# Performance work log

Hardware: AMD Instinct MI355X
Metric: run time of the kernel (lower is better)

Reference implementation:

```python
import jax, jax.numpy as jnp
import numpy as np

N, E, D, L = 50000, 800000, 64, 4
ATOM_VOCAB, BOND_VOCAB, N_ATOM_F, N_BOND_F = 64, 8, 9, 3
BN_EPS = 1e-5


def _bn_train(z, g, b):
    # BatchNorm1d in training mode: batch mean, biased variance
    mu = jnp.mean(z, axis=0)
    var = jnp.mean((z - mu) ** 2, axis=0)
    return (z - mu) * jax.lax.rsqrt(var + BN_EPS) * g + b


def _multi_embed(tables, idx):
    # tables: [F, V, D], idx: [N, F] -> sum over F of tables[f][idx[:, f]] -> [N, D]
    return jax.vmap(lambda t, c: t[c], in_axes=(0, 1))(tables, idx).sum(0)


def setup_inputs() -> dict:
    key = jax.random.key(0)
    ks = jax.random.split(key, 8)
    s = 0.1
    return {
        "x": jax.random.randint(ks[0], (N, N_ATOM_F), 0, ATOM_VOCAB),
        "edge_index": jax.random.randint(ks[1], (2, E), 0, N),
        "edge_attr": jax.random.randint(ks[2], (E, N_BOND_F), 0, BOND_VOCAB),
        "atom_emb": jax.random.normal(ks[3], (N_ATOM_F, ATOM_VOCAB, D), jnp.float32) * s,
        "bond_emb": jax.random.normal(ks[4], (L, N_BOND_F, BOND_VOCAB, D), jnp.float32) * s,
        "lin1_w": jax.random.normal(ks[5], (L, D, 2 * D), jnp.float32) * s,
        "lin1_b": jnp.zeros((L, 2 * D), jnp.float32),
        "bn1_g": jnp.ones((L, 2 * D), jnp.float32),
        "bn1_b": jnp.zeros((L, 2 * D), jnp.float32),
        "lin2_w": jax.random.normal(ks[6], (L, 2 * D, D), jnp.float32) * s,
        "lin2_b": jnp.zeros((L, D), jnp.float32),
        "eps": jnp.zeros((L,), jnp.float32),
        "bn_g": jnp.ones((L, D), jnp.float32),
        "bn_b": jnp.zeros((L, D), jnp.float32),
    }


def reference(x, edge_index, edge_attr, atom_emb, bond_emb, lin1_w, lin1_b,
              bn1_g, bn1_b, lin2_w, lin2_b, eps, bn_g, bn_b):
    n_nodes = x.shape[0]
    n_layers = lin1_w.shape[0]
    src, dst = edge_index[0], edge_index[1]
    # AtomEncoder: sum of per-feature embeddings
    h = _multi_embed(atom_emb, x)  # [N, D]
    for l in range(n_layers):
        e = _multi_embed(bond_emb[l], edge_attr)  # [E, D] bond encoding
        msg = jax.nn.relu(h[src] + e)  # gather + elementwise message
        agg = jax.ops.segment_sum(msg, dst, num_segments=n_nodes)  # scatter-add
        z = (1.0 + eps[l]) * h + agg  # GIN update
        z = jax.nn.relu(_bn_train(z @ lin1_w[l] + lin1_b[l], bn1_g[l], bn1_b[l]))
        z = z @ lin2_w[l] + lin2_b[l]
        h = _bn_train(z, bn_g[l], bn_b[l])  # outer BatchNorm
        if l < n_layers - 1:
            h = jax.nn.relu(h)
    return h  # JK='last' node representation [N, D]
```

## Files before the change

kernel.cpp:

```cpp
#include <hip/hip_runtime.h>
#include <hip/hip_bf16.h>

#define NN 50000
#define NE 800000
#define NAF 9
#define NBF 3
#define BN_EPS 1e-5f
#define NBUK 196
#define CHUNK 8192
#define NTILE 3125
#define MMB 1563

typedef __attribute__((ext_vector_type(8))) short bf16x8;
typedef __attribute__((ext_vector_type(4))) float f32x4;

__device__ __forceinline__ short f2b(float f) {
  unsigned u = __float_as_uint(f);
  unsigned r = (u + 0x7FFFu + ((u >> 16) & 1u)) >> 16;
  return (short)r;
}

__device__ __forceinline__ float b2f(unsigned short v) {
  return __uint_as_float(((unsigned)v) << 16);
}

__device__ __forceinline__ bf16x8 pack8(float4 a, float4 b) {
  bf16x8 v;
  v[0] = f2b(a.x); v[1] = f2b(a.y); v[2] = f2b(a.z); v[3] = f2b(a.w);
  v[4] = f2b(b.x); v[5] = f2b(b.y); v[6] = f2b(b.z); v[7] = f2b(b.w);
  return v;
}

__global__ __launch_bounds__(256) void k_atom(const int* __restrict__ x,
                                              const float* __restrict__ aemb,
                                              float* __restrict__ h,
                                              unsigned short* __restrict__ hb) {
  int node = (blockIdx.x * 256 + threadIdx.x) >> 6;
  int lane = threadIdx.x & 63;
  if (node >= NN) return;
  const int* xr = x + node * NAF;
  float acc = 0.f;
#pragma unroll
  for (int f = 0; f < NAF; ++f) acc += aemb[(f * 64 + xr[f]) * 64 + lane];
  h[(size_t)node * 64 + lane] = acc;
  hb[(size_t)node * 64 + lane] = (unsigned short)f2b(acc);
}

__global__ __launch_bounds__(256) void k_prep(const float* __restrict__ w1,
                                              const float* __restrict__ w2,
                                              bf16x8* __restrict__ pre1,
                                              bf16x8* __restrict__ pre2) {
  int f = (blockIdx.x & 15) * 256 + threadIdx.x;
  int lane = f & 63, c = lane & 15, g = lane >> 4;
  if (blockIdx.x < 16) {
    int kh = (f >> 6) & 1, t = (f >> 7) & 7, l = f >> 10;
    const float* w = w1 + (size_t)l * 64 * 128;
    bf16x8 v;
#pragma unroll
    for (int j = 0; j < 8; ++j) v[j] = f2b(w[(kh * 32 + g * 8 + j) * 128 + t * 16 + c]);
    pre1[f] = v;
  } else {
    int kf = (f >> 6) & 3, t = (f >> 8) & 3, l = f >> 10;
    const float* w = w2 + (size_t)l * 128 * 64;
    bf16x8 v;
#pragma unroll
    for (int j = 0; j < 8; ++j) v[j] = f2b(w[(kf * 32 + g * 8 + j) * 64 + t * 16 + c]);
    pre2[f] = v;
  }
}

__global__ __launch_bounds__(256) void k_red(const float* __restrict__ partial,
                                             float* __restrict__ st, int width) {
  int col = threadIdx.x;
  if (col >= width) return;
  int per = (MMB + gridDim.x - 1) / gridDim.x;
  int r0 = blockIdx.x * per;
  int r1 = min(MMB, r0 + per);
  float s = 0.f;
  int r = r0;
  for (; r + 4 <= r1; r += 4) {
    s += partial[(size_t)r * width + col] + partial[(size_t)(r + 1) * width + col]
       + partial[(size_t)(r + 2) * width + col] + partial[(size_t)(r + 3) * width + col];
  }
  for (; r < r1; ++r) s += partial[(size_t)r * width + col];
  atomicAdd(&st[col], s);
}

__global__ __launch_bounds__(256) void k_hprep(float* __restrict__ zB,
                                               const float* __restrict__ st,
                                               const float* __restrict__ g,
                                               const float* __restrict__ b,
                                               unsigned short* __restrict__ hb) {
  __shared__ float ns[64], nbv[64];
  if (threadIdx.x < 64) {
    int c = threadIdx.x;
    const float inv = 1.0f / NN;
    float mu = st[c] * inv;
    float var = st[64 + c] * inv - mu * mu;
    float sc = rsqrtf(var + BN_EPS) * g[c];
    ns[c] = sc;
    nbv[c] = b[c] - mu * sc;
  }
  __syncthreads();
  float4* z4 = (float4*)zB;
  ushort4* hb4 = (ushort4*)hb;
  int total = NN * 16;
  for (int i = blockIdx.x * 256 + threadIdx.x; i < total; i += gridDim.x * 256) {
    float4 v = z4[i];
    int c = (i & 15) * 4;
    v.x = fmaxf(fmaf(v.x, ns[c], nbv[c]), 0.f);
    v.y = fmaxf(fmaf(v.y, ns[c + 1], nbv[c + 1]), 0.f);
    v.z = fmaxf(fmaf(v.z, ns[c + 2], nbv[c + 2]), 0.f);
    v.w = fmaxf(fmaf(v.w, ns[c + 3], nbv[c + 3]), 0.f);
    z4[i] = v;
    ushort4 o;
    o.x = (unsigned short)f2b(v.x);
    o.y = (unsigned short)f2b(v.y);
    o.z = (unsigned short)f2b(v.z);
    o.w = (unsigned short)f2b(v.w);
    hb4[i] = o;
  }
}

__global__ __launch_bounds__(1024) void k_pack_hist(const int* __restrict__ ei,
                                                    const int* __restrict__ ea,
                                                    uint2* __restrict__ pairs,
                                                    int* __restrict__ counts,
                                                    int* __restrict__ bcnt) {
  __shared__ int lh[NBUK];
  for (int i = threadIdx.x; i < NBUK; i += 1024) lh[i] = 0;
  __syncthreads();
  for (int e = blockIdx.x * 1024 + threadIdx.x; e < NE; e += gridDim.x * 1024) {
    int src = ei[e];
    int dst = ei[NE + e];
    unsigned code = (unsigned)(ea[e * 3] | (ea[e * 3 + 1] << 3) | (ea[e * 3 + 2] << 6));
    pairs[e] = make_uint2((unsigned)src | (code << 17), (unsigned)dst);
    atomicAdd(&counts[dst], 1);
    atomicAdd(&lh[dst >> 8], 1);
  }
  __syncthreads();
  for (int i = threadIdx.x; i < NBUK; i += 1024)
    if (lh[i]) atomicAdd(&bcnt[i], lh[i]);
}

__global__ __launch_bounds__(256) void k_scanb(const int* __restrict__ bcnt,
                                               int* __restrict__ bbase,
                                               int* __restrict__ bfill) {
  int tid = threadIdx.x;
  int c = (tid < NBUK) ? bcnt[tid] : 0;
  int lane = tid & 63, wid = tid >> 6;
  int inc = c;
#pragma unroll
  for (int off = 1; off < 64; off <<= 1) {
    int t = __shfl_up(inc, off);
    if (lane >= off) inc += t;
  }
  __shared__ int wt[4];
  if (lane == 63) wt[wid] = inc;
  __syncthreads();
  int woff = 0;
#pragma unroll
  for (int w = 0; w < 4; ++w) woff += (w < wid) ? wt[w] : 0;
  if (tid < NBUK) { int e = inc - c + woff; bbase[tid] = e; bfill[tid] = e; }
}

__global__ __launch_bounds__(256) void k_scan1(const int* __restrict__ counts,
                                               int* __restrict__ row_ptr,
                                               int* __restrict__ bsum) {
  int tid = threadIdx.x;
  int node = blockIdx.x * 256 + tid;
  int c = (node < NN) ? counts[node] : 0;
  int lane = tid & 63, wid = tid >> 6;
  int inc = c;
#pragma unroll
  for (int off = 1; off < 64; off <<= 1) {
    int t = __shfl_up(inc, off);
    if (lane >= off) inc += t;
  }
  __shared__ int wt[4];
  if (lane == 63) wt[wid] = inc;
  __syncthreads();
  int woff = 0;
#pragma unroll
  for (int w = 0; w < 4; ++w) woff += (w < wid) ? wt[w] : 0;
  if (node < NN) row_ptr[node] = inc - c + woff;
  if (tid == 255) bsum[blockIdx.x] = woff + inc;
}

__global__ __launch_bounds__(256) void k_scan2(const int* __restrict__ bsum,
                                               int* __restrict__ boff, int nb) {
  int tid = threadIdx.x;
  int c = (tid < nb) ? bsum[tid] : 0;
  int lane = tid & 63, wid = tid >> 6;
  int inc = c;
#pragma unroll
  for (int off = 1; off < 64; off <<= 1) {
    int t = __shfl_up(inc, off);
    if (lane >= off) inc += t;
  }
  __shared__ int wt[4];
  if (lane == 63) wt[wid] = inc;
  __syncthreads();
  int woff = 0;
#pragma unroll
  for (int w = 0; w < 4; ++w) woff += (w < wid) ? wt[w] : 0;
  if (tid < nb) boff[tid] = inc - c + woff;
}

__global__ __launch_bounds__(256) void k_scan3(int* __restrict__ row_ptr,
                                               const int* __restrict__ boff) {
  int node = blockIdx.x * 256 + threadIdx.x;
  if (node < NN) row_ptr[node] += boff[blockIdx.x];
  if (node == 0) row_ptr[NN] = NE;
}

__global__ __launch_bounds__(1024) void k_bin(const uint2* __restrict__ pairs,
                                              int* __restrict__ bfill,
                                              uint2* __restrict__ binned) {
  __shared__ uint2 st[CHUNK];
  __shared__ int lh[NBUK];
  __shared__ int gbase[NBUK];
  int tid = threadIdx.x;
  int base = blockIdx.x * CHUNK;
  int n = NE - base; if (n > CHUNK) n = CHUNK;
  for (int i = tid; i < NBUK; i += 1024) lh[i] = 0;
  __syncthreads();
  for (int i = tid; i < n; i += 1024) {
    uint2 p = pairs[base + i];
    st[i] = p;
    atomicAdd(&lh[p.y >> 8], 1);
  }
  __syncthreads();
  for (int i = tid; i < NBUK; i += 1024) {
    int c = lh[i];
    gbase[i] = c ? atomicAdd(&bfill[i], c) : 0;
  }
  __syncthreads();
  for (int i = tid; i < NBUK; i += 1024) lh[i] = 0;
  __syncthreads();
  for (int i = tid; i < n; i += 1024) {
    uint2 p = st[i];
    int b = p.y >> 8;
    int r = atomicAdd(&lh[b], 1);
    binned[gbase[b] + r] = p;
  }
}

__global__ __launch_bounds__(1024) void k_fin(const uint2* __restrict__ binned,
                                              const int* __restrict__ bbase,
                                              const int* __restrict__ bcnt,
                                              const int* __restrict__ row_ptr,
                                              unsigned* __restrict__ epack) {
  __shared__ int cur[256];
  int b = blockIdx.x;
  int tid = threadIdx.x;
  int node0 = b << 8;
  if (tid < 256) cur[tid] = (node0 + tid < NN) ? row_ptr[node0 + tid] : 0;
  __syncthreads();
  int s = bbase[b], n = bcnt[b];
  for (int i = tid; i < n; i += 1024) {
    uint2 p = binned[s + i];
    int pos = atomicAdd(&cur[p.y & 255], 1);
    epack[pos] = p.x;
  }
}

__global__ __launch_bounds__(256) void k_agg(const float* __restrict__ hf,
                                             const unsigned short* __restrict__ hb,
                                             const float* __restrict__ bemb,
                                             const float* __restrict__ eps, int l,
                                             const int* __restrict__ row_ptr,
                                             const unsigned* __restrict__ epack,
                                             float* __restrict__ z) {
  __shared__ float tab[NBF * 8 * 64];
  const float* bt = bemb + (size_t)l * NBF * 8 * 64;
  for (int i = threadIdx.x; i < NBF * 8 * 64; i += 256) tab[i] = bt[i];
  __syncthreads();
  const float4* tab4 = (const float4*)tab;
  const ushort4* hb4 = (const ushort4*)hb;
  const float4* hf4 = (const float4*)hf;

  int node = (blockIdx.x * 256 + threadIdx.x) >> 6;
  int lane = threadIdx.x & 63;
  if (node >= NN) return;
  int gr = lane >> 4;
  int c4 = lane & 15;

  int beg = row_ptr[node], end = row_ptr[node + 1];
  float4 acc = {0.f, 0.f, 0.f, 0.f};

  auto edge = [&](unsigned p, ushort4 hv) {
    unsigned cd = p >> 17;
    float4 ea_ = tab4[(cd & 7) * 16 + c4];
    float4 eb_ = tab4[128 + ((cd >> 3) & 7) * 16 + c4];
    float4 ec_ = tab4[256 + ((cd >> 6) & 7) * 16 + c4];
    acc.x += fmaxf(b2f(hv.x) + ea_.x + eb_.x + ec_.x, 0.f);
    acc.y += fmaxf(b2f(hv.y) + ea_.y + eb_.y + ec_.y, 0.f);
    acc.z += fmaxf(b2f(hv.z) + ea_.z + eb_.z + ec_.z, 0.f);
    acc.w += fmaxf(b2f(hv.w) + ea_.w + eb_.w + ec_.w, 0.f);
  };

  int i = beg + gr;
  for (; i + 12 < end; i += 16) {
    unsigned p0 = epack[i];
    unsigned p1 = epack[i + 4];
    unsigned p2 = epack[i + 8];
    unsigned p3 = epack[i + 12];
    ushort4 h0 = hb4[(size_t)(p0 & 0x1FFFFu) * 16 + c4];
    ushort4 h1 = hb4[(size_t)(p1 & 0x1FFFFu) * 16 + c4];
    ushort4 h2 = hb4[(size_t)(p2 & 0x1FFFFu) * 16 + c4];
    ushort4 h3 = hb4[(size_t)(p3 & 0x1FFFFu) * 16 + c4];
    edge(p0, h0); edge(p1, h1); edge(p2, h2); edge(p3, h3);
  }
  for (; i < end; i += 4) {
    unsigned p0 = epack[i];
    ushort4 h0 = hb4[(size_t)(p0 & 0x1FFFFu) * 16 + c4];
    edge(p0, h0);
  }
#pragma unroll
  for (int off = 16; off <= 32; off <<= 1) {
    acc.x += __shfl_xor(acc.x, off);
    acc.y += __shfl_xor(acc.y, off);
    acc.z += __shfl_xor(acc.z, off);
    acc.w += __shfl_xor(acc.w, off);
  }
  if (gr == 0) {
    float4 self = hf4[(size_t)node * 16 + c4];
    float se = 1.0f + eps[l];
    float4 out;
    out.x = fmaf(self.x, se, acc.x);
    out.y = fmaf(self.y, se, acc.y);
    out.z = fmaf(self.z, se, acc.z);
    out.w = fmaf(self.w, se, acc.w);
    ((float4*)z)[(size_t)node * 16 + c4] = out;
  }
}

__global__ __launch_bounds__(256) void k_mm1(const float* __restrict__ z,
                                             const bf16x8* __restrict__ pre1,
                                             const float* __restrict__ b1,
                                             int l, float* __restrict__ y,
                                             float* __restrict__ part1) {
  __shared__ float lz[2][16 * 68];
  int tid = threadIdx.x;
  int lane = tid & 63;
  int wid = tid >> 6;
  int c = lane & 15;
  int g = lane >> 4;

  int t0 = blockIdx.x * 2;
  int ntl = (t0 + 1 < NTILE) ? 2 : 1;

  const float4* zt = (const float4*)(z + (size_t)t0 * 16 * 64);
  int nf4 = ntl * 256;
  for (int i = tid; i < nf4; i += 256) {
    float4 v = zt[i];
    int tile = i >> 8;
    int f4 = i & 255;
    int row = f4 >> 4, c4i = f4 & 15;
    *(float4*)(&lz[tile][row * 68 + c4i * 4]) = v;
  }

  bf16x8 Bf[2][2];
#pragma unroll
  for (int u = 0; u < 2; ++u)
#pragma unroll
    for (int kh = 0; kh < 2; ++kh)
      Bf[u][kh] = pre1[(((size_t)l * 8 + wid * 2 + u) * 2 + kh) * 64 + lane];
  float bias0 = b1[l * 128 + (wid * 2) * 16 + c];
  float bias1 = b1[l * 128 + (wid * 2 + 1) * 16 + c];

  __syncthreads();

  float ssum0 = 0.f, ssum1 = 0.f, sq0 = 0.f, sq1 = 0.f;

#pragma unroll
  for (int u = 0; u < 2; ++u) {
    if (u >= ntl) break;
    int rowbase = (t0 + u) * 16;
    const float* myz = lz[u];
    float4 q0 = *(const float4*)(myz + c * 68 + g * 8);
    float4 q1 = *(const float4*)(myz + c * 68 + g * 8 + 4);
    float4 q2 = *(const float4*)(myz + c * 68 + 32 + g * 8);
    float4 q3 = *(const float4*)(myz + c * 68 + 32 + g * 8 + 4);
    bf16x8 a0 = pack8(q0, q1);
    bf16x8 a1 = pack8(q2, q3);

    f32x4 acc0 = {bias0, bias0, bias0, bias0};
    acc0 = __builtin_amdgcn_mfma_f32_16x16x32_bf16(a0, Bf[0][0], acc0, 0, 0, 0);
    acc0 = __builtin_amdgcn_mfma_f32_16x16x32_bf16(a1, Bf[0][1], acc0, 0, 0, 0);
    f32x4 acc1 = {bias1, bias1, bias1, bias1};
    acc1 = __builtin_amdgcn_mfma_f32_16x16x32_bf16(a0, Bf[1][0], acc1, 0, 0, 0);
    acc1 = __builtin_amdgcn_mfma_f32_16x16x32_bf16(a1, Bf[1][1], acc1, 0, 0, 0);

    int tc0 = wid * 2, tc1 = wid * 2 + 1;
#pragma unroll
    for (int r = 0; r < 4; ++r) {
      float v0 = acc0[r], v1 = acc1[r];
      y[(size_t)(rowbase + g * 4 + r) * 128 + tc0 * 16 + c] = v0;
      y[(size_t)(rowbase + g * 4 + r) * 128 + tc1 * 16 + c] = v1;
      ssum0 += v0; sq0 = fmaf(v0, v0, sq0);
      ssum1 += v1; sq1 = fmaf(v1, v1, sq1);
    }
  }
  ssum0 += __shfl_xor(ssum0, 16); ssum0 += __shfl_xor(ssum0, 32);
  ssum1 += __shfl_xor(ssum1, 16); ssum1 += __shfl_xor(ssum1, 32);
  sq0 += __shfl_xor(sq0, 16); sq0 += __shfl_xor(sq0, 32);
  sq1 += __shfl_xor(sq1, 16); sq1 += __shfl_xor(sq1, 32);
  if (g == 0) {
    float* pp = part1 + (size_t)blockIdx.x * 256;
    pp[(wid * 2) * 16 + c] = ssum0;
    pp[(wid * 2 + 1) * 16 + c] = ssum1;
    pp[128 + (wid * 2) * 16 + c] = sq0;
    pp[128 + (wid * 2 + 1) * 16 + c] = sq1;
  }
}

__global__ __launch_bounds__(256) void k_mm2(const float* __restrict__ y,
                                             const bf16x8* __restrict__ pre2,
                                             const float* __restrict__ b2,
                                             const float* __restrict__ g1,
                                             const float* __restrict__ bb1,
                                             int l, float* __restrict__ z2,
                                             const float* __restrict__ st1,
                                             float* __restrict__ part2) {
  __shared__ float ly[2][16 * 132];
  __shared__ float ns[128], nb[128];
  int tid = threadIdx.x;
  int lane = tid & 63;
  int wid = tid >> 6;
  int c = lane & 15;
  int g = lane >> 4;

  int t0 = blockIdx.x * 2;
  int ntl = (t0 + 1 < NTILE) ? 2 : 1;

  const float4* yt = (const float4*)(y + (size_t)t0 * 16 * 128);
  int nf4 = ntl * 512;
  for (int i = tid; i < nf4; i += 256) {
    float4 v = yt[i];
    int tile = i >> 9;
    int f4 = i & 511;
    int row = f4 >> 5, c4i = f4 & 31;
    *(float4*)(&ly[tile][row * 132 + c4i * 4]) = v;
  }

  if (tid < 128) {
    int ch = tid;
    const float inv = 1.0f / NN;
    float mu = st1[ch] * inv;
    float var = st1[128 + ch] * inv - mu * mu;
    float sc = rsqrtf(var + BN_EPS) * g1[l * 128 + ch];
    ns[ch] = sc;
    nb[ch] = bb1[l * 128 + ch] - mu * sc;
  }

  bf16x8 Bf[4];
#pragma unroll
  for (int kf = 0; kf < 4; ++kf)
    Bf[kf] = pre2[(((size_t)l * 4 + wid) * 4 + kf) * 64 + lane];
  float bias = b2[l * 64 + wid * 16 + c];

  __syncthreads();

  const float4* nsf = (const float4*)ns;
  const float4* nbf = (const float4*)nb;
  float ssum = 0.f, sq = 0.f;

#pragma unroll
  for (int u = 0; u < 2; ++u) {
    if (u >= ntl) break;
    int rowbase = (t0 + u) * 16;
    const float* myy = ly[u];
    bf16x8 A[4];
#pragma unroll
    for (int kf = 0; kf < 4; ++kf) {
      float4 q0 = *(const float4*)(myy + c * 132 + kf * 32 + g * 8);
      float4 q1 = *(const float4*)(myy + c * 132 + kf * 32 + g * 8 + 4);
      float4 s0 = nsf[kf * 8 + g * 2];
      float4 s1 = nsf[kf * 8 + g * 2 + 1];
      float4 o0 = nbf[kf * 8 + g * 2];
      float4 o1 = nbf[kf * 8 + g * 2 + 1];
      float4 v0, v1;
      v0.x = fmaxf(fmaf(q0.x, s0.x, o0.x), 0.f);
      v0.y = fmaxf(fmaf(q0.y, s0.y, o0.y), 0.f);
      v0.z = fmaxf(fmaf(q0.z, s0.z, o0.z), 0.f);
      v0.w = fmaxf(fmaf(q0.w, s0.w, o0.w), 0.f);
      v1.x = fmaxf(fmaf(q1.x, s1.x, o1.x), 0.f);
      v1.y = fmaxf(fmaf(q1.y, s1.y, o1.y), 0.f);
      v1.z = fmaxf(fmaf(q1.z, s1.z, o1.z), 0.f);
      v1.w = fmaxf(fmaf(q1.w, s1.w, o1.w), 0.f);
      A[kf] = pack8(v0, v1);
    }
    f32x4 acc = {bias, bias, bias, bias};
#pragma unroll
    for (int kf = 0; kf < 4; ++kf)
      acc = __builtin_amdgcn_mfma_f32_16x16x32_bf16(A[kf], Bf[kf], acc, 0, 0, 0);
#pragma unroll
    for (int r = 0; r < 4; ++r) {
      float v = acc[r];
      z2[(size_t)(rowbase + g * 4 + r) * 64 + wid * 16 + c] = v;
      ssum += v; sq = fmaf(v, v, sq);
    }
  }
  ssum += __shfl_xor(ssum, 16); ssum += __shfl_xor(ssum, 32);
  sq += __shfl_xor(sq, 16); sq += __shfl_xor(sq, 32);
  if (g == 0) {
    float* pp = part2 + (size_t)blockIdx.x * 128;
    pp[wid * 16 + c] = ssum;
    pp[64 + wid * 16 + c] = sq;
  }
}

__global__ __launch_bounds__(256) void k_bn2(const float* __restrict__ z2,
                                             const float* __restrict__ g,
                                             const float* __restrict__ b,
                                             const float* __restrict__ st,
                                             float* __restrict__ h) {
  __shared__ float ns[64], nb[64];
  if (threadIdx.x < 64) {
    int c = threadIdx.x;
    const float inv = 1.0f / NN;
    float mu = st[c] * inv;
    float var = st[64 + c] * inv - mu * mu;
    float sc = rsqrtf(var + BN_EPS) * g[c];
    ns[c] = sc;
    nb[c] = b[c] - mu * sc;
  }
  __syncthreads();
  const float4* zin = (const float4*)z2;
  float4* hout = (float4*)h;
  int total = NN * 16;
  for (int i = blockIdx.x * 256 + threadIdx.x; i < total; i += gridDim.x * 256) {
    float4 v = zin[i];
    int c = (i & 15) * 4;
    v.x = fmaf(v.x, ns[c], nb[c]);
    v.y = fmaf(v.y, ns[c + 1], nb[c + 1]);
    v.z = fmaf(v.z, ns[c + 2], nb[c + 2]);
    v.w = fmaf(v.w, ns[c + 3], nb[c + 3]);
    hout[i] = v;
  }
}

extern "C" void kernel_launch(void* const* d_in, const int* in_sizes, int n_in,
                              void* d_out, int out_size, void* d_ws, size_t ws_size,
                              hipStream_t stream) {
  const int* x = (const int*)d_in[0];
  const int* ei = (const int*)d_in[1];
  const int* ea = (const int*)d_in[2];
  const float* aemb = (const float*)d_in[3];
  const float* bemb = (const float*)d_in[4];
  const float* l1w = (const float*)d_in[5];
  const float* l1b = (const float*)d_in[6];
  const float* g1 = (const float*)d_in[7];
  const float* bb1 = (const float*)d_in[8];
  const float* l2w = (const float*)d_in[9];
  const float* l2b = (const float*)d_in[10];
  const float* eps = (const float*)d_in[11];
  const float* bng = (const float*)d_in[12];
  const float* bnb = (const float*)d_in[13];
  float* out = (float*)d_out;

  char* p = (char*)d_ws;
  float* zA = (float*)p;           p += (size_t)NN * 64 * 4;
  float* y = (float*)p;            p += (size_t)NN * 128 * 4;
  float* zB = (float*)p;           p += (size_t)NN * 64 * 4;
  unsigned* epack = (unsigned*)p;  p += (size_t)NE * 4;
  int* row_ptr = (int*)p;          p += (size_t)(NN + 1) * 4;
  int* counts = (int*)p;           p += (size_t)NN * 4;
  int* bcnt = (int*)p;             p += 256 * 4;
  int* bbase = (int*)p;            p += 256 * 4;
  int* bfill = (int*)p;            p += 256 * 4;
  float* stats = (float*)p;        p += 4 * 384 * 4;
  int* bsum = (int*)p;             p += 256 * 4;
  int* boff = (int*)p;             p += 256 * 4;
  bf16x8* pre1 = (bf16x8*)p;       p += 4096 * 16;
  bf16x8* pre2 = (bf16x8*)p;       p += 4096 * 16;
  float* part1 = (float*)p;        p += (size_t)MMB * 256 * 4;
  float* part2 = (float*)p;        p += (size_t)MMB * 128 * 4;

  uint2* pairs = (uint2*)zA;
  uint2* binned = (uint2*)y;
  unsigned short* hb = (unsigned short*)y;
  float* h0 = zB;

  const int NB = (NN + 255) / 256;

  hipMemsetAsync(counts, 0, (size_t)NN * 4, stream);
  hipMemsetAsync(bcnt, 0, 256 * 4, stream);
  hipMemsetAsync(stats, 0, 4 * 384 * 4, stream);

  k_prep<<<32, 256, 0, stream>>>(l1w, l2w, pre1, pre2);
  k_pack_hist<<<256, 1024, 0, stream>>>(ei, ea, pairs, counts, bcnt);
  k_scanb<<<1, 256, 0, stream>>>(bcnt, bbase, bfill);
  k_scan1<<<NB, 256, 0, stream>>>(counts, row_ptr, bsum);
  k_scan2<<<1, 256, 0, stream>>>(bsum, boff, NB);
  k_scan3<<<NB, 256, 0, stream>>>(row_ptr, boff);
  k_bin<<<(NE + CHUNK - 1) / CHUNK, 1024, 0, stream>>>(pairs, bfill, binned);
  k_fin<<<NBUK, 1024, 0, stream>>>(binned, bbase, bcnt, row_ptr, epack);

  k_atom<<<NN / 4, 256, 0, stream>>>(x, aemb, h0, hb);

  for (int l = 0; l < 4; ++l) {
    float* st1 = stats + l * 384;
    float* st2 = st1 + 256;
    if (l > 0) {
      const float* stp = stats + (l - 1) * 384 + 256;
      k_hprep<<<1024, 256, 0, stream>>>(zB, stp, bng + (l - 1) * 64,
                                        bnb + (l - 1) * 64, hb);
    }
    k_agg<<<NN / 4, 256, 0, stream>>>(zB, hb, bemb, eps, l, row_ptr, epack, zA);
    k_mm1<<<MMB, 256, 0, stream>>>(zA, pre1, l1b, l, y, part1);
    k_red<<<32, 256, 0, stream>>>(part1, st1, 256);
    k_mm2<<<MMB, 256, 0, stream>>>(y, pre2, l2b, g1, bb1, l, zB, st1, part2);
    k_red<<<32, 256, 0, stream>>>(part2, st2, 128);
  }
  k_bn2<<<1024, 256, 0, stream>>>(zB, bng + 3 * 64, bnb + 3 * 64,
                                  stats + 3 * 384 + 256, out);
}
```

Measured before the change: 417.9 us.

## Fuse CSR build into bucket kernels and precombine bond embedding tables

The CSR construction is restructured. A histogram kernel now counts only coarse buckets. Packing the edges is folded into the binning kernel, and each bucket's finalize kernel computes its per-node counts and exclusive scan locally. This removes the global per-node atomic counts, the three-pass scan, the counts memset and the intermediate pairs buffer. Separately, the aggregation kernel precomputes a padded 64-entry table holding the sum of the first two bond feature embeddings, so each edge does two LDS lookups instead of three. The cost is a second pass over the binned edges in the finalize kernel and an edge-index read in both hist and bin.

```diff
diff --git a/kernel.cpp b/kernel.cpp
--- a/kernel.cpp
+++ b/kernel.cpp
@@ -122,24 +122,15 @@
   }
 }
 
-__global__ __launch_bounds__(1024) void k_pack_hist(const int* __restrict__ ei,
-                                                    const int* __restrict__ ea,
-                                                    uint2* __restrict__ pairs,
-                                                    int* __restrict__ counts,
-                                                    int* __restrict__ bcnt) {
+__global__ __launch_bounds__(256) void k_hist2(const int* __restrict__ ei,
+                                               int* __restrict__ bcnt) {
   __shared__ int lh[NBUK];
-  for (int i = threadIdx.x; i < NBUK; i += 1024) lh[i] = 0;
-  __syncthreads();
-  for (int e = blockIdx.x * 1024 + threadIdx.x; e < NE; e += gridDim.x * 1024) {
-    int src = ei[e];
-    int dst = ei[NE + e];
-    unsigned code = (unsigned)(ea[e * 3] | (ea[e * 3 + 1] << 3) | (ea[e * 3 + 2] << 6));
-    pairs[e] = make_uint2((unsigned)src | (code << 17), (unsigned)dst);
-    atomicAdd(&counts[dst], 1);
-    atomicAdd(&lh[dst >> 8], 1);
-  }
-  __syncthreads();
-  for (int i = threadIdx.x; i < NBUK; i += 1024)
+  for (int i = threadIdx.x; i < NBUK; i += 256) lh[i] = 0;
+  __syncthreads();
+  for (int e = blockIdx.x * 256 + threadIdx.x; e < NE; e += gridDim.x * 256)
+    atomicAdd(&lh[ei[NE + e] >> 8], 1);
+  __syncthreads();
+  for (int i = threadIdx.x; i < NBUK; i += 256)
     if (lh[i]) atomicAdd(&bcnt[i], lh[i]);
 }
 
@@ -164,59 +155,10 @@
   if (tid < NBUK) { int e = inc - c + woff; bbase[tid] = e; bfill[tid] = e; }
 }
 
-__global__ __launch_bounds__(256) void k_scan1(const int* __restrict__ counts,
-                                               int* __restrict__ row_ptr,
-                                               int* __restrict__ bsum) {
-  int tid = threadIdx.x;
-  int node = blockIdx.x * 256 + tid;
-  int c = (node < NN) ? counts[node] : 0;
-  int lane = tid & 63, wid = tid >> 6;
-  int inc = c;
-#pragma unroll
-  for (int off = 1; off < 64; off <<= 1) {
-    int t = __shfl_up(inc, off);
-    if (lane >= off) inc += t;
-  }
-  __shared__ int wt[4];
-  if (lane == 63) wt[wid] = inc;
-  __syncthreads();
-  int woff = 0;
-#pragma unroll
-  for (int w = 0; w < 4; ++w) woff += (w < wid) ? wt[w] : 0;
-  if (node < NN) row_ptr[node] = inc - c + woff;
-  if (tid == 255) bsum[blockIdx.x] = woff + inc;
-}
-
-__global__ __launch_bounds__(256) void k_scan2(const int* __restrict__ bsum,
-                                               int* __restrict__ boff, int nb) {
-  int tid = threadIdx.x;
-  int c = (tid < nb) ? bsum[tid] : 0;
-  int lane = tid & 63, wid = tid >> 6;
-  int inc = c;
-#pragma unroll
-  for (int off = 1; off < 64; off <<= 1) {
-    int t = __shfl_up(inc, off);
-    if (lane >= off) inc += t;
-  }
-  __shared__ int wt[4];
-  if (lane == 63) wt[wid] = inc;
-  __syncthreads();
-  int woff = 0;
-#pragma unroll
-  for (int w = 0; w < 4; ++w) woff += (w < wid) ? wt[w] : 0;
-  if (tid < nb) boff[tid] = inc - c + woff;
-}
-
-__global__ __launch_bounds__(256) void k_scan3(int* __restrict__ row_ptr,
-                                               const int* __restrict__ boff) {
-  int node = blockIdx.x * 256 + threadIdx.x;
-  if (node < NN) row_ptr[node] += boff[blockIdx.x];
-  if (node == 0) row_ptr[NN] = NE;
-}
-
-__global__ __launch_bounds__(1024) void k_bin(const uint2* __restrict__ pairs,
-                                              int* __restrict__ bfill,
-                                              uint2* __restrict__ binned) {
+__global__ __launch_bounds__(1024) void k_bin2(const int* __restrict__ ei,
+                                               const int* __restrict__ ea,
+                                               int* __restrict__ bfill,
+                                               uint2* __restrict__ binned) {
   __shared__ uint2 st[CHUNK];
   __shared__ int lh[NBUK];
   __shared__ int gbase[NBUK];
@@ -226,9 +168,12 @@
   for (int i = tid; i < NBUK; i += 1024) lh[i] = 0;
   __syncthreads();
   for (int i = tid; i < n; i += 1024) {
-    uint2 p = pairs[base + i];
-    st[i] = p;
-    atomicAdd(&lh[p.y >> 8], 1);
+    int e = base + i;
+    int src = ei[e];
+    int dst = ei[NE + e];
+    unsigned code = (unsigned)(ea[e * 3] | (ea[e * 3 + 1] << 3) | (ea[e * 3 + 2] << 6));
+    st[i] = make_uint2((unsigned)src | (code << 17), (unsigned)dst);
+    atomicAdd(&lh[dst >> 8], 1);
   }
   __syncthreads();
   for (int i = tid; i < NBUK; i += 1024) {
@@ -246,18 +191,44 @@
   }
 }
 
-__global__ __launch_bounds__(1024) void k_fin(const uint2* __restrict__ binned,
-                                              const int* __restrict__ bbase,
-                                              const int* __restrict__ bcnt,
-                                              const int* __restrict__ row_ptr,
-                                              unsigned* __restrict__ epack) {
+__global__ __launch_bounds__(1024) void k_finAll(const uint2* __restrict__ binned,
+                                                 const int* __restrict__ bbase,
+                                                 const int* __restrict__ bcnt,
+                                                 int* __restrict__ row_ptr,
+                                                 unsigned* __restrict__ epack) {
+  __shared__ int cnt[256];
   __shared__ int cur[256];
-  int b = blockIdx.x;
-  int tid = threadIdx.x;
-  int node0 = b << 8;
-  if (tid < 256) cur[tid] = (node0 + tid < NN) ? row_ptr[node0 + tid] : 0;
+  __shared__ int wt[4];
+  int b = blockIdx.x, tid = threadIdx.x;
+  if (tid < 256) cnt[tid] = 0;
   __syncthreads();
   int s = bbase[b], n = bcnt[b];
+  for (int i = tid; i < n; i += 1024) atomicAdd(&cnt[binned[s + i].y & 255], 1);
+  __syncthreads();
+  int lane = tid & 63, w = tid >> 6;
+  int c = 0, inc = 0;
+  if (tid < 256) {
+    c = cnt[tid];
+    inc = c;
+#pragma unroll
+    for (int off = 1; off < 64; off <<= 1) {
+      int t = __shfl_up(inc, off);
+      if (lane >= off) inc += t;
+    }
+    if (lane == 63) wt[w] = inc;
+  }
+  __syncthreads();
+  if (tid < 256) {
+    int woff = 0;
+#pragma unroll
+    for (int i = 0; i < 4; ++i) woff += (i < w) ? wt[i] : 0;
+    int excl = s + inc - c + woff;
+    int node = (b << 8) + tid;
+    if (node < NN) row_ptr[node] = excl;
+    cur[tid] = excl;
+  }
+  if (b == NBUK - 1 && tid == 0) row_ptr[NN] = NE;
+  __syncthreads();
   for (int i = tid; i < n; i += 1024) {
     uint2 p = binned[s + i];
     int pos = atomicAdd(&cur[p.y & 255], 1);
@@ -272,11 +243,23 @@
                                              const int* __restrict__ row_ptr,
                                              const unsigned* __restrict__ epack,
                                              float* __restrict__ z) {
-  __shared__ float tab[NBF * 8 * 64];
+  __shared__ float t12[64 * 68];
+  __shared__ float t3[8 * 68];
   const float* bt = bemb + (size_t)l * NBF * 8 * 64;
-  for (int i = threadIdx.x; i < NBF * 8 * 64; i += 256) tab[i] = bt[i];
-  __syncthreads();
-  const float4* tab4 = (const float4*)tab;
+  const float4* bt4 = (const float4*)bt;
+  for (int i = threadIdx.x; i < 64 * 16; i += 256) {
+    int combo = i >> 4, ch4 = i & 15;
+    float4 a = bt4[(combo & 7) * 16 + ch4];
+    float4 b = bt4[128 + (combo >> 3) * 16 + ch4];
+    float4 sum;
+    sum.x = a.x + b.x; sum.y = a.y + b.y; sum.z = a.z + b.z; sum.w = a.w + b.w;
+    *(float4*)(t12 + combo * 68 + ch4 * 4) = sum;
+  }
+  for (int i = threadIdx.x; i < 8 * 16; i += 256) {
+    int row = i >> 4, ch4 = i & 15;
+    *(float4*)(t3 + row * 68 + ch4 * 4) = bt4[256 + row * 16 + ch4];
+  }
+  __syncthreads();
   const ushort4* hb4 = (const ushort4*)hb;
   const float4* hf4 = (const float4*)hf;
 
@@ -291,13 +274,12 @@
 
   auto edge = [&](unsigned p, ushort4 hv) {
     unsigned cd = p >> 17;
-    float4 ea_ = tab4[(cd & 7) * 16 + c4];
-    float4 eb_ = tab4[128 + ((cd >> 3) & 7) * 16 + c4];
-    float4 ec_ = tab4[256 + ((cd >> 6) & 7) * 16 + c4];
-    acc.x += fmaxf(b2f(hv.x) + ea_.x + eb_.x + ec_.x, 0.f);
-    acc.y += fmaxf(b2f(hv.y) + ea_.y + eb_.y + ec_.y, 0.f);
-    acc.z += fmaxf(b2f(hv.z) + ea_.z + eb_.z + ec_.z, 0.f);
-    acc.w += fmaxf(b2f(hv.w) + ea_.w + eb_.w + ec_.w, 0.f);
+    float4 e12 = *(const float4*)(t12 + (cd & 63) * 68 + c4 * 4);
+    float4 e3 = *(const float4*)(t3 + (cd >> 6) * 68 + c4 * 4);
+    acc.x += fmaxf(b2f(hv.x) + e12.x + e3.x, 0.f);
+    acc.y += fmaxf(b2f(hv.y) + e12.y + e3.y, 0.f);
+    acc.z += fmaxf(b2f(hv.z) + e12.z + e3.z, 0.f);
+    acc.w += fmaxf(b2f(hv.w) + e12.w + e3.w, 0.f);
   };
 
   int i = beg + gr;
@@ -567,37 +549,27 @@
   float* zB = (float*)p;           p += (size_t)NN * 64 * 4;
   unsigned* epack = (unsigned*)p;  p += (size_t)NE * 4;
   int* row_ptr = (int*)p;          p += (size_t)(NN + 1) * 4;
-  int* counts = (int*)p;           p += (size_t)NN * 4;
   int* bcnt = (int*)p;             p += 256 * 4;
   int* bbase = (int*)p;            p += 256 * 4;
   int* bfill = (int*)p;            p += 256 * 4;
   float* stats = (float*)p;        p += 4 * 384 * 4;
-  int* bsum = (int*)p;             p += 256 * 4;
-  int* boff = (int*)p;             p += 256 * 4;
   bf16x8* pre1 = (bf16x8*)p;       p += 4096 * 16;
   bf16x8* pre2 = (bf16x8*)p;       p += 4096 * 16;
   float* part1 = (float*)p;        p += (size_t)MMB * 256 * 4;
   float* part2 = (float*)p;        p += (size_t)MMB * 128 * 4;
 
-  uint2* pairs = (uint2*)zA;
   uint2* binned = (uint2*)y;
   unsigned short* hb = (unsigned short*)y;
   float* h0 = zB;
 
-  const int NB = (NN + 255) / 256;
-
-  hipMemsetAsync(counts, 0, (size_t)NN * 4, stream);
   hipMemsetAsync(bcnt, 0, 256 * 4, stream);
   hipMemsetAsync(stats, 0, 4 * 384 * 4, stream);
 
   k_prep<<<32, 256, 0, stream>>>(l1w, l2w, pre1, pre2);
-  k_pack_hist<<<256, 1024, 0, stream>>>(ei, ea, pairs, counts, bcnt);
+  k_hist2<<<256, 256, 0, stream>>>(ei, bcnt);
   k_scanb<<<1, 256, 0, stream>>>(bcnt, bbase, bfill);
-  k_scan1<<<NB, 256, 0, stream>>>(counts, row_ptr, bsum);
-  k_scan2<<<1, 256, 0, stream>>>(bsum, boff, NB);
-  k_scan3<<<NB, 256, 0, stream>>>(row_ptr, boff);
-  k_bin<<<(NE + CHUNK - 1) / CHUNK, 1024, 0, stream>>>(pairs, bfill, binned);
-  k_fin<<<NBUK, 1024, 0, stream>>>(binned, bbase, bcnt, row_ptr, epack);
+  k_bin2<<<(NE + CHUNK - 1) / CHUNK, 1024, 0, stream>>>(ei, ea, bfill, binned);
+  k_finAll<<<NBUK, 1024, 0, stream>>>(binned, bbase, bcnt, row_ptr, epack);
 
   k_atom<<<NN / 4, 256, 0, stream>>>(x, aemb, h0, hb);
 
```

Measured after the change: 382.8 us. 8.4% less time.
